# Optimization experiments

Hardware: AMD Instinct MI355X
Metric: run time of the kernel (lower is better)

Reference implementation:

```python
import jax, jax.numpy as jnp
import numpy as np

N = 50000
E = 600000
D_IN = 128
D_OUT = 128
EPS = 1e-12  # F.normalize eps


def setup_inputs() -> dict:
    key = jax.random.key(0)
    ks = jax.random.split(key, 10)
    s = 1.0 / np.sqrt(D_IN)
    inp = {
        "x": jax.random.normal(ks[0], (N, D_IN), dtype=jnp.float32),
        "edge_index": jax.random.randint(ks[1], (2, E), 0, N, dtype=jnp.int64),
        # conv1: lin_l (with bias) applied to aggregated neighbors, lin_r (no bias) to root
        "W1l": jax.random.uniform(ks[2], (D_IN, D_IN), jnp.float32, -s, s),
        "b1": jax.random.uniform(ks[3], (D_IN,), jnp.float32, -s, s),
        "W1r": jax.random.uniform(ks[4], (D_IN, D_IN), jnp.float32, -s, s),
        # conv2
        "W2l": jax.random.uniform(ks[5], (D_IN, D_OUT), jnp.float32, -s, s),
        "b2": jax.random.uniform(ks[6], (D_OUT,), jnp.float32, -s, s),
        "W2r": jax.random.uniform(ks[7], (D_IN, D_OUT), jnp.float32, -s, s),
        # final fc
        "Wf": jax.random.uniform(ks[8], (D_OUT, D_OUT), jnp.float32, -s, s),
        "bf": jax.random.uniform(ks[9], (D_OUT,), jnp.float32, -s, s),
    }
    return inp


def _sage_conv(x, src, dst, Wl, bl, Wr):
    # mean-aggregate messages from source nodes onto destination nodes
    msgs = x[src]  # [E, d] gather
    agg = jax.ops.segment_sum(msgs, dst, num_segments=N)  # [N, d]
    cnt = jax.ops.segment_sum(jnp.ones((src.shape[0],), x.dtype), dst, num_segments=N)
    agg = agg / jnp.maximum(cnt, 1.0)[:, None]  # isolated nodes -> 0
    out = agg @ Wl + bl + x @ Wr
    # L2 normalize per node (PyG normalize=True)
    nrm = jnp.sqrt(jnp.sum(out * out, axis=-1, keepdims=True))
    return out / jnp.maximum(nrm, EPS)


def reference(x, edge_index, W1l, b1, W1r, W2l, b2, W2r, Wf, bf):
    src, dst = edge_index[0], edge_index[1]
    h = jax.nn.relu(_sage_conv(x, src, dst, W1l, b1, W1r))
    h = jax.nn.relu(_sage_conv(h, src, dst, W2l, b2, W2r))
    return h @ Wf + bf
```

## Files before the change

### kernel.cpp

```cpp
#include <hip/hip_runtime.h>
#include <hip/hip_fp16.h>

#define D 128
#define SCAN_B 256

typedef __attribute__((ext_vector_type(8))) _Float16 f16x8;
typedef __attribute__((ext_vector_type(4))) float f32x4;

typedef __attribute__((address_space(1))) const void gas_t;
typedef __attribute__((address_space(3))) void las_t;

__global__ void scan_pass1(const int* __restrict__ cnt, int* __restrict__ rs,
                           int* __restrict__ bsum, int N) {
    __shared__ int lds[SCAN_B];
    int tid = threadIdx.x;
    int i = blockIdx.x * SCAN_B + tid;
    int v = (i < N) ? cnt[i] : 0;
    lds[tid] = v;
    __syncthreads();
    for (int o = 1; o < SCAN_B; o <<= 1) {
        int t = (tid >= o) ? lds[tid - o] : 0;
        __syncthreads();
        lds[tid] += t;
        __syncthreads();
    }
    if (i < N) rs[i] = lds[tid] - v;
    if (tid == SCAN_B - 1) bsum[blockIdx.x] = lds[tid];
}

__global__ void scan_pass2(int* __restrict__ bsum, int nb) {
    __shared__ int lds[SCAN_B];
    int tid = threadIdx.x;
    int v = (tid < nb) ? bsum[tid] : 0;
    lds[tid] = v;
    __syncthreads();
    for (int o = 1; o < SCAN_B; o <<= 1) {
        int t = (tid >= o) ? lds[tid - o] : 0;
        __syncthreads();
        lds[tid] += t;
        __syncthreads();
    }
    if (tid < nb) bsum[tid] = lds[tid] - v;
}

__global__ void scan_pass3(int* __restrict__ rs, int* __restrict__ cursor,
                           const int* __restrict__ bsum, const int* __restrict__ cnt,
                           float* __restrict__ inv, int N) {
    int i = blockIdx.x * SCAN_B + threadIdx.x;
    if (i < N) {
        int v = rs[i] + bsum[blockIdx.x];
        rs[i] = v;
        cursor[i] = v;
        inv[i] = 1.0f / (float)max(cnt[i], 1);
    }
}

__global__ void fill_kernel(const int* __restrict__ ei, int E,
                            int* __restrict__ cursor, int* __restrict__ csr) {
    int e = blockIdx.x * blockDim.x + threadIdx.x;
    if (e < E) {
        int src = ei[e], dst = ei[E + e];
        int pos = atomicAdd(&cursor[dst], 1);
        csr[pos] = src;
    }
}

__global__ void prologue_kernel(const float* __restrict__ W1l, const float* __restrict__ W1r,
                                const float* __restrict__ W2l, const float* __restrict__ W2r,
                                const float* __restrict__ Wf, unsigned short* __restrict__ pw,
                                const float* __restrict__ x, __half* __restrict__ xh,
                                __half* __restrict__ xl, int n8,
                                const int* __restrict__ ei, int E, int* __restrict__ cnt) {
    int t = blockIdx.x * blockDim.x + threadIdx.x;
    if (t < 10240) {
        int idx = t;
        int w = idx >> 11;
        int r = idx & 2047;
        int ks = r >> 9;
        int tt = (r >> 6) & 7;
        int lane = r & 63;
        int q = lane >> 4, n = lane & 15;
        const float* W = (w == 0) ? W1l : (w == 1) ? W1r : (w == 2) ? W2l : (w == 3) ? W2r : Wf;
        unsigned short* dh = pw + (size_t)w * 32768;
        unsigned short* dl = dh + 16384;
        int off = ((ks * 8 + tt) * 64 + lane) * 8;
#pragma unroll
        for (int j = 0; j < 8; j++) {
            float v = W[(size_t)(ks * 32 + q * 8 + j) * D + tt * 16 + n];
            __half hb = __float2half_rn(v);
            dh[off + j] = __half_as_ushort(hb);
            dl[off + j] = __half_as_ushort(__float2half_rn(v - __half2float(hb)));
        }
    } else if (t < 10240 + n8) {
        int i = t - 10240;
        const float4* x4 = (const float4*)x;
        float4 a = x4[2 * i], b = x4[2 * i + 1];
        float v[8] = {a.x, a.y, a.z, a.w, b.x, b.y, b.z, b.w};
        uint4 oh, ol;
        __half2* ph = (__half2*)&oh;
        __half2* pl = (__half2*)&ol;
#pragma unroll
        for (int jj = 0; jj < 4; jj++) {
            __half h0 = __float2half_rn(v[2 * jj]);
            __half h1 = __float2half_rn(v[2 * jj + 1]);
            ph[jj] = __halves2half2(h0, h1);
            pl[jj] = __halves2half2(__float2half_rn(v[2 * jj] - __half2float(h0)),
                                    __float2half_rn(v[2 * jj + 1] - __half2float(h1)));
        }
        ((uint4*)xh)[i] = oh;
        ((uint4*)xl)[i] = ol;
    } else {
        int e = t - 10240 - n8;
        if (e < E) atomicAdd(&cnt[ei[E + e]], 1);
    }
}

__device__ __forceinline__ void acc8(uint4 v, float* s) {
    const __half2* h = reinterpret_cast<const __half2*>(&v);
    float2 f0 = __half22float2(h[0]);
    float2 f1 = __half22float2(h[1]);
    float2 f2 = __half22float2(h[2]);
    float2 f3 = __half22float2(h[3]);
    s[0] += f0.x; s[1] += f0.y; s[2] += f1.x; s[3] += f1.y;
    s[4] += f2.x; s[5] += f2.y; s[6] += f3.x; s[7] += f3.y;
}

__global__ void aggregate_kernel(const __half* __restrict__ xh, int sstride,
                                 const int* __restrict__ csr,
                                 const int* __restrict__ rs, const int* __restrict__ cnt,
                                 const float* __restrict__ inv,
                                 __half* __restrict__ aggh, __half* __restrict__ aggl, int N) {
    int t = blockIdx.x * blockDim.x + threadIdx.x;
    int node = t >> 4;
    int c = t & 15;
    if (node >= N) return;
    int deg = cnt[node];
    int st = rs[node];
    const uint4* x4 = (const uint4*)xh;
    float s[8] = {0.f, 0.f, 0.f, 0.f, 0.f, 0.f, 0.f, 0.f};
    int i = 0;
    for (; i + 4 <= deg; i += 4) {
        int n0 = csr[st + i + 0], n1 = csr[st + i + 1];
        int n2 = csr[st + i + 2], n3 = csr[st + i + 3];
        uint4 v0 = x4[(size_t)n0 * sstride + c];
        uint4 v1 = x4[(size_t)n1 * sstride + c];
        uint4 v2 = x4[(size_t)n2 * sstride + c];
        uint4 v3 = x4[(size_t)n3 * sstride + c];
        acc8(v0, s); acc8(v1, s); acc8(v2, s); acc8(v3, s);
    }
    for (; i < deg; i++) {
        int n0 = csr[st + i];
        uint4 v0 = x4[(size_t)n0 * sstride + c];
        acc8(v0, s);
    }
    float iv = inv[node];
    uint4 oh, ol;
    __half2* ph = (__half2*)&oh;
    __half2* pl = (__half2*)&ol;
#pragma unroll
    for (int jj = 0; jj < 4; jj++) {
        float v0 = s[2 * jj] * iv, v1 = s[2 * jj + 1] * iv;
        __half h0 = __float2half_rn(v0), h1 = __float2half_rn(v1);
        ph[jj] = __halves2half2(h0, h1);
        pl[jj] = __halves2half2(__float2half_rn(v0 - __half2float(h0)),
                                __float2half_rn(v1 - __half2float(h1)));
    }
    ((uint4*)aggh)[(size_t)node * 16 + c] = oh;
    ((uint4*)aggl)[(size_t)node * 16 + c] = ol;
}

template <int LAYER>
__global__ __launch_bounds__(256) void mfma_gemm(
        const uint4* __restrict__ Agh, const uint4* __restrict__ Agl,
        const uint4* __restrict__ Ah1, const uint4* __restrict__ Al1,
        const uint4* __restrict__ W0h, const uint4* __restrict__ W0l,
        const uint4* __restrict__ W1h, const uint4* __restrict__ W1l,
        const float* __restrict__ bias,
        const uint4* __restrict__ W2h, const uint4* __restrict__ W2l,
        const float* __restrict__ bias2,
        float* out, __half* Hout, int N) {
    __shared__ uint4 smem4[2048];

    const int tid = threadIdx.x;
    const int lane = tid & 63;
    const int wave = tid >> 6;
    const int c = lane & 15;
    const int q = lane >> 4;
    const int R = blockIdx.x * 64 + wave * 16;
    const int row0 = min(R + c, N - 1);
    const size_t rb16 = (size_t)row0 * 16 + q;
    const size_t rbA1 = (size_t)row0 * (LAYER == 1 ? 16 : 32) + q;

#define STAGE_W(ks_, b_)                                                                   \
    do {                                                                                   \
        const uint4* sh_ = (((ks_) < 4) ? W0h : W1h) + (size_t)((ks_) & 3) * 512;          \
        const uint4* sl_ = (((ks_) < 4) ? W0l : W1l) + (size_t)((ks_) & 3) * 512;          \
        const uint4* s_ = ((wave < 2) ? sh_ : sl_) + ((wave & 1) * 256 + lane);            \
        uint4* d_ = smem4 + (b_) * 1024 + (wave >> 1) * 512 + (wave & 1) * 256;            \
        __builtin_amdgcn_global_load_lds((gas_t*)(s_), (las_t*)(d_), 16, 0, 0);            \
        __builtin_amdgcn_global_load_lds((gas_t*)(s_ + 64), (las_t*)(d_ + 64), 16, 0, 0);  \
        __builtin_amdgcn_global_load_lds((gas_t*)(s_ + 128), (las_t*)(d_ + 128), 16, 0, 0);\
        __builtin_amdgcn_global_load_lds((gas_t*)(s_ + 192), (las_t*)(d_ + 192), 16, 0, 0);\
    } while (0)

#define LOAD_A(ks_, s_)                                                       \
    do {                                                                      \
        if ((ks_) < 4) {                                                      \
            A_h[s_] = Agh[rb16 + (ks_) * 4];                                  \
            A_l[s_] = Agl[rb16 + (ks_) * 4];                                  \
        } else {                                                              \
            A_h[s_] = Ah1[rbA1 + ((ks_) - 4) * 4];                            \
            A_l[s_] = Al1[rbA1 + ((ks_) - 4) * 4];                            \
        }                                                                     \
    } while (0)

    uint4 A_h[2], A_l[2];
    STAGE_W(0, 0);
    STAGE_W(1, 1);
    LOAD_A(0, 0);
    LOAD_A(1, 1);
    asm volatile("s_waitcnt vmcnt(0)" ::: "memory");
    __syncthreads();

    f32x4 acc[8];
#pragma unroll
    for (int t = 0; t < 8; t++)
#pragma unroll
        for (int r = 0; r < 4; r++) acc[t][r] = 0.0f;

#pragma unroll
    for (int ks = 0; ks < 8; ks++) {
        const int b = ks & 1;
        const uint4* wb = smem4 + b * 1024;
        f16x8 ah = __builtin_bit_cast(f16x8, A_h[b]);
        f16x8 al = __builtin_bit_cast(f16x8, A_l[b]);
#pragma unroll
        for (int t = 0; t < 8; t++) {
            f16x8 bh = __builtin_bit_cast(f16x8, wb[t * 64 + lane]);
            f16x8 bl = __builtin_bit_cast(f16x8, wb[512 + t * 64 + lane]);
            acc[t] = __builtin_amdgcn_mfma_f32_16x16x32_f16(ah, bh, acc[t], 0, 0, 0);
            acc[t] = __builtin_amdgcn_mfma_f32_16x16x32_f16(al, bh, acc[t], 0, 0, 0);
            acc[t] = __builtin_amdgcn_mfma_f32_16x16x32_f16(ah, bl, acc[t], 0, 0, 0);
        }
        if (ks < 7) {
            asm volatile("s_waitcnt vmcnt(0)" ::: "memory");
            __syncthreads();
            if (ks < 6) {
                STAGE_W(ks + 2, b);
                LOAD_A(ks + 2, b);
            }
        }
    }

#pragma unroll
    for (int t = 0; t < 8; t++) {
        float bv = bias[t * 16 + c];
#pragma unroll
        for (int r = 0; r < 4; r++) acc[t][r] += bv;
    }
#pragma unroll
    for (int r = 0; r < 4; r++) {
        float v = 0.0f;
#pragma unroll
        for (int t = 0; t < 8; t++) v += acc[t][r] * acc[t][r];
        v += __shfl_xor(v, 1, 16);
        v += __shfl_xor(v, 2, 16);
        v += __shfl_xor(v, 4, 16);
        v += __shfl_xor(v, 8, 16);
        float rn = 1.0f / fmaxf(sqrtf(v), 1e-12f);
#pragma unroll
        for (int t = 0; t < 8; t++) acc[t][r] = fmaxf(acc[t][r] * rn, 0.0f);
    }

    if (LAYER == 1) {
#pragma unroll
        for (int t = 0; t < 8; t++)
#pragma unroll
            for (int r = 0; r < 4; r++) {
                int row = R + q * 4 + r;
                if (row < N) {
                    float v = acc[t][r];
                    __half h = __float2half_rn(v);
                    size_t base = (size_t)row * 256;
                    Hout[base + t * 16 + c] = h;
                    Hout[base + 128 + t * 16 + c] = __float2half_rn(v - __half2float(h));
                }
            }
        return;
    }

    __syncthreads();
    unsigned short* hw = (unsigned short*)(smem4 + wave * 512);
#pragma unroll
    for (int t = 0; t < 8; t++)
#pragma unroll
        for (int r = 0; r < 4; r++) {
            int m = q * 4 + r;
            float v = acc[t][r];
            __half h = __float2half_rn(v);
            int j4 = (t * 2 + (c >> 3)) ^ (m & 7);
            int off = m * 128 + j4 * 8 + (c & 7);
            hw[off] = __half_as_ushort(h);
            hw[2048 + off] = __half_as_ushort(__float2half_rn(v - __half2float(h)));
        }
    uint4 a2h_[4], a2l_[4];
#pragma unroll
    for (int k2 = 0; k2 < 4; k2++) {
        int r4 = (k2 * 4 + q) ^ (c & 7);
        a2h_[k2] = *(const uint4*)(hw + c * 128 + r4 * 8);
        a2l_[k2] = *(const uint4*)(hw + 2048 + c * 128 + r4 * 8);
    }

    f32x4 acc2[8];
#pragma unroll
    for (int t = 0; t < 8; t++) {
        float bv = bias2[t * 16 + c];
#pragma unroll
        for (int r = 0; r < 4; r++) acc2[t][r] = bv;
    }
#pragma unroll
    for (int k2 = 0; k2 < 4; k2++) {
        const uint4* Wh = W2h + (size_t)k2 * 512 + lane;
        const uint4* Wl = W2l + (size_t)k2 * 512 + lane;
        f16x8 ah = __builtin_bit_cast(f16x8, a2h_[k2]);
        f16x8 al = __builtin_bit_cast(f16x8, a2l_[k2]);
#pragma unroll
        for (int t = 0; t < 8; t++) {
            f16x8 bh = __builtin_bit_cast(f16x8, Wh[t * 64]);
            f16x8 bl = __builtin_bit_cast(f16x8, Wl[t * 64]);
            acc2[t] = __builtin_amdgcn_mfma_f32_16x16x32_f16(ah, bh, acc2[t], 0, 0, 0);
            acc2[t] = __builtin_amdgcn_mfma_f32_16x16x32_f16(al, bh, acc2[t], 0, 0, 0);
            acc2[t] = __builtin_amdgcn_mfma_f32_16x16x32_f16(ah, bl, acc2[t], 0, 0, 0);
        }
    }

#pragma unroll
    for (int t = 0; t < 8; t++)
#pragma unroll
        for (int r = 0; r < 4; r++) {
            int row = R + q * 4 + r;
            if (row < N) out[(size_t)row * D + t * 16 + c] = acc2[t][r];
        }
#undef STAGE_W
#undef LOAD_A
}

extern "C" void kernel_launch(void* const* d_in, const int* in_sizes, int n_in,
                              void* d_out, int out_size, void* d_ws, size_t ws_size,
                              hipStream_t stream) {
    const float* x   = (const float*)d_in[0];
    const int*   ei  = (const int*)d_in[1];
    const float* W1l = (const float*)d_in[2];
    const float* b1  = (const float*)d_in[3];
    const float* W1r = (const float*)d_in[4];
    const float* W2l = (const float*)d_in[5];
    const float* b2  = (const float*)d_in[6];
    const float* W2r = (const float*)d_in[7];
    const float* Wf  = (const float*)d_in[8];
    const float* bf  = (const float*)d_in[9];
    float* out = (float*)d_out;

    int N = in_sizes[0] / D;
    int E = in_sizes[1] / 2;

    __half* Agh = (__half*)d_ws;
    __half* Agl = Agh + (size_t)N * D;
    __half* Xh  = Agl + (size_t)N * D;
    __half* Xl  = Xh + (size_t)N * D;
    float* inv  = (float*)(Xl + (size_t)N * D);
    int*   rs     = (int*)(inv + N);
    int*   cnt    = rs + N;
    int*   cursor = cnt + N;
    int*   bsum   = cursor + N;
    int*   csr    = bsum + 256;
    unsigned short* pw = (unsigned short*)(csr + E);
    unsigned short* p1lh = pw + 0 * 32768, *p1ll = p1lh + 16384;
    unsigned short* p1rh = pw + 1 * 32768, *p1rl = p1rh + 16384;
    unsigned short* p2lh = pw + 2 * 32768, *p2ll = p2lh + 16384;
    unsigned short* p2rh = pw + 3 * 32768, *p2rl = p2rh + 16384;
    unsigned short* pfh  = pw + 4 * 32768, *pfl  = pfh + 16384;

    __half* H1 = (__half*)d_out;

    int nb = (N + SCAN_B - 1) / SCAN_B;
    int n8 = N * 16;

    hipMemsetAsync(cnt, 0, (size_t)N * sizeof(int), stream);
    int pro_threads = 10240 + n8 + E;
    prologue_kernel<<<(pro_threads + 255) / 256, 256, 0, stream>>>(
        W1l, W1r, W2l, W2r, Wf, pw, x, Xh, Xl, n8, ei, E, cnt);
    scan_pass1<<<nb, SCAN_B, 0, stream>>>(cnt, rs, bsum, N);
    scan_pass2<<<1, SCAN_B, 0, stream>>>(bsum, nb);
    scan_pass3<<<nb, SCAN_B, 0, stream>>>(rs, cursor, bsum, cnt, inv, N);
    fill_kernel<<<(E + 255) / 256, 256, 0, stream>>>(ei, E, cursor, csr);

    int agg_blocks = (N * 16 + 255) / 256;
    int gemm_blocks = (N + 63) / 64;

    aggregate_kernel<<<agg_blocks, 256, 0, stream>>>(Xh, 16, csr, rs, cnt, inv, Agh, Agl, N);
    mfma_gemm<1><<<gemm_blocks, 256, 0, stream>>>(
        (const uint4*)Agh, (const uint4*)Agl, (const uint4*)Xh, (const uint4*)Xl,
        (const uint4*)p1lh, (const uint4*)p1ll, (const uint4*)p1rh, (const uint4*)p1rl, b1,
        nullptr, nullptr, nullptr, nullptr, H1, N);

    aggregate_kernel<<<agg_blocks, 256, 0, stream>>>(H1, 32, csr, rs, cnt, inv, Agh, Agl, N);
    mfma_gemm<2><<<gemm_blocks, 256, 0, stream>>>(
        (const uint4*)Agh, (const uint4*)Agl,
        (const uint4*)d_out, (const uint4*)d_out + 16,
        (const uint4*)p2lh, (const uint4*)p2ll, (const uint4*)p2rh, (const uint4*)p2rl, b2,
        (const uint4*)pfh, (const uint4*)pfl, bf, out, nullptr, N);
}
```

Baseline: 261.0 us.

## Fuse neighbor mean aggregation into the MFMA GEMM kernels

Removes the separate aggregate kernels and instead has each GEMM lane gather and average its row's neighbor features directly into registers, split into hi/lo fp16, before the MFMA loop. This drops the write and re-read of the aggregated Agh/Agl buffers and two kernel launches. H1 moves from the output buffer into workspace. The trade-off is that each node's gather is now spread over only 4 lanes per row with 16-byte strided loads, leaving far fewer threads for the irregular gather. It also raises register pressure, because 32 float accumulators plus 16 uint4 operands are held per lane.

```diff
diff --git a/kernel.cpp b/kernel.cpp
--- a/kernel.cpp
+++ b/kernel.cpp
@@ -125,53 +125,24 @@
     s[4] += f2.x; s[5] += f2.y; s[6] += f3.x; s[7] += f3.y;
 }
 
-__global__ void aggregate_kernel(const __half* __restrict__ xh, int sstride,
-                                 const int* __restrict__ csr,
-                                 const int* __restrict__ rs, const int* __restrict__ cnt,
-                                 const float* __restrict__ inv,
-                                 __half* __restrict__ aggh, __half* __restrict__ aggl, int N) {
-    int t = blockIdx.x * blockDim.x + threadIdx.x;
-    int node = t >> 4;
-    int c = t & 15;
-    if (node >= N) return;
-    int deg = cnt[node];
-    int st = rs[node];
-    const uint4* x4 = (const uint4*)xh;
-    float s[8] = {0.f, 0.f, 0.f, 0.f, 0.f, 0.f, 0.f, 0.f};
-    int i = 0;
-    for (; i + 4 <= deg; i += 4) {
-        int n0 = csr[st + i + 0], n1 = csr[st + i + 1];
-        int n2 = csr[st + i + 2], n3 = csr[st + i + 3];
-        uint4 v0 = x4[(size_t)n0 * sstride + c];
-        uint4 v1 = x4[(size_t)n1 * sstride + c];
-        uint4 v2 = x4[(size_t)n2 * sstride + c];
-        uint4 v3 = x4[(size_t)n3 * sstride + c];
-        acc8(v0, s); acc8(v1, s); acc8(v2, s); acc8(v3, s);
-    }
-    for (; i < deg; i++) {
-        int n0 = csr[st + i];
-        uint4 v0 = x4[(size_t)n0 * sstride + c];
-        acc8(v0, s);
-    }
-    float iv = inv[node];
-    uint4 oh, ol;
-    __half2* ph = (__half2*)&oh;
-    __half2* pl = (__half2*)&ol;
+__device__ __forceinline__ void split_f16(const float* v, uint4& hi, uint4& lo) {
+    __half2* ph = (__half2*)&hi;
+    __half2* pl = (__half2*)&lo;
 #pragma unroll
     for (int jj = 0; jj < 4; jj++) {
-        float v0 = s[2 * jj] * iv, v1 = s[2 * jj + 1] * iv;
-        __half h0 = __float2half_rn(v0), h1 = __float2half_rn(v1);
+        __half h0 = __float2half_rn(v[2 * jj]);
+        __half h1 = __float2half_rn(v[2 * jj + 1]);
         ph[jj] = __halves2half2(h0, h1);
-        pl[jj] = __halves2half2(__float2half_rn(v0 - __half2float(h0)),
-                                __float2half_rn(v1 - __half2float(h1)));
-    }
-    ((uint4*)aggh)[(size_t)node * 16 + c] = oh;
-    ((uint4*)aggl)[(size_t)node * 16 + c] = ol;
+        pl[jj] = __halves2half2(__float2half_rn(v[2 * jj] - __half2float(h0)),
+                                __float2half_rn(v[2 * jj + 1] - __half2float(h1)));
+    }
 }
 
 template <int LAYER>
-__global__ __launch_bounds__(256) void mfma_gemm(
-        const uint4* __restrict__ Agh, const uint4* __restrict__ Agl,
+__global__ __launch_bounds__(256) void fused_gemm(
+        const int* __restrict__ csr, const int* __restrict__ rs,
+        const int* __restrict__ cnt, const float* __restrict__ inv,
+        const uint4* __restrict__ Gsrc,
         const uint4* __restrict__ Ah1, const uint4* __restrict__ Al1,
         const uint4* __restrict__ W0h, const uint4* __restrict__ W0l,
         const uint4* __restrict__ W1h, const uint4* __restrict__ W1l,
@@ -180,6 +151,7 @@
         const float* __restrict__ bias2,
         float* out, __half* Hout, int N) {
     __shared__ uint4 smem4[2048];
+    const int GS = (LAYER == 1) ? 16 : 32;
 
     const int tid = threadIdx.x;
     const int lane = tid & 63;
@@ -188,8 +160,7 @@
     const int q = lane >> 4;
     const int R = blockIdx.x * 64 + wave * 16;
     const int row0 = min(R + c, N - 1);
-    const size_t rb16 = (size_t)row0 * 16 + q;
-    const size_t rbA1 = (size_t)row0 * (LAYER == 1 ? 16 : 32) + q;
+    const size_t rbA1 = (size_t)row0 * GS + q;
 
 #define STAGE_W(ks_, b_)                                                                   \
     do {                                                                                   \
@@ -203,22 +174,50 @@
         __builtin_amdgcn_global_load_lds((gas_t*)(s_ + 192), (las_t*)(d_ + 192), 16, 0, 0);\
     } while (0)
 
-#define LOAD_A(ks_, s_)                                                       \
-    do {                                                                      \
-        if ((ks_) < 4) {                                                      \
-            A_h[s_] = Agh[rb16 + (ks_) * 4];                                  \
-            A_l[s_] = Agl[rb16 + (ks_) * 4];                                  \
-        } else {                                                              \
-            A_h[s_] = Ah1[rbA1 + ((ks_) - 4) * 4];                            \
-            A_l[s_] = Al1[rbA1 + ((ks_) - 4) * 4];                            \
-        }                                                                     \
-    } while (0)
-
-    uint4 A_h[2], A_l[2];
     STAGE_W(0, 0);
     STAGE_W(1, 1);
-    LOAD_A(0, 0);
-    LOAD_A(1, 1);
+    uint4 Xs_h[4], Xs_l[4];
+#pragma unroll
+    for (int kl = 0; kl < 4; kl++) {
+        Xs_h[kl] = Ah1[rbA1 + kl * 4];
+        Xs_l[kl] = Al1[rbA1 + kl * 4];
+    }
+
+    int deg = cnt[row0];
+    int st = rs[row0];
+    float iv = inv[row0];
+    float s[4][8];
+#pragma unroll
+    for (int ks = 0; ks < 4; ks++)
+#pragma unroll
+        for (int j = 0; j < 8; j++) s[ks][j] = 0.0f;
+
+    int i = 0;
+    for (; i + 2 <= deg; i += 2) {
+        int n0 = csr[st + i], n1 = csr[st + i + 1];
+        const uint4* g0 = Gsrc + (size_t)n0 * GS + q;
+        const uint4* g1 = Gsrc + (size_t)n1 * GS + q;
+        uint4 a0 = g0[0], a1 = g0[4], a2 = g0[8], a3 = g0[12];
+        uint4 b0 = g1[0], b1 = g1[4], b2 = g1[8], b3 = g1[12];
+        acc8(a0, s[0]); acc8(a1, s[1]); acc8(a2, s[2]); acc8(a3, s[3]);
+        acc8(b0, s[0]); acc8(b1, s[1]); acc8(b2, s[2]); acc8(b3, s[3]);
+    }
+    if (i < deg) {
+        int n0 = csr[st + i];
+        const uint4* g0 = Gsrc + (size_t)n0 * GS + q;
+        uint4 a0 = g0[0], a1 = g0[4], a2 = g0[8], a3 = g0[12];
+        acc8(a0, s[0]); acc8(a1, s[1]); acc8(a2, s[2]); acc8(a3, s[3]);
+    }
+
+    uint4 Agg_h[4], Agg_l[4];
+#pragma unroll
+    for (int ks = 0; ks < 4; ks++) {
+        float v[8];
+#pragma unroll
+        for (int j = 0; j < 8; j++) v[j] = s[ks][j] * iv;
+        split_f16(v, Agg_h[ks], Agg_l[ks]);
+    }
+
     asm volatile("s_waitcnt vmcnt(0)" ::: "memory");
     __syncthreads();
 
@@ -232,8 +231,8 @@
     for (int ks = 0; ks < 8; ks++) {
         const int b = ks & 1;
         const uint4* wb = smem4 + b * 1024;
-        f16x8 ah = __builtin_bit_cast(f16x8, A_h[b]);
-        f16x8 al = __builtin_bit_cast(f16x8, A_l[b]);
+        f16x8 ah = __builtin_bit_cast(f16x8, (ks < 4) ? Agg_h[ks & 3] : Xs_h[ks & 3]);
+        f16x8 al = __builtin_bit_cast(f16x8, (ks < 4) ? Agg_l[ks & 3] : Xs_l[ks & 3]);
 #pragma unroll
         for (int t = 0; t < 8; t++) {
             f16x8 bh = __builtin_bit_cast(f16x8, wb[t * 64 + lane]);
@@ -245,10 +244,7 @@
         if (ks < 7) {
             asm volatile("s_waitcnt vmcnt(0)" ::: "memory");
             __syncthreads();
-            if (ks < 6) {
-                STAGE_W(ks + 2, b);
-                LOAD_A(ks + 2, b);
-            }
+            if (ks < 6) STAGE_W(ks + 2, b);
         }
     }
 
@@ -342,7 +338,6 @@
             if (row < N) out[(size_t)row * D + t * 16 + c] = acc2[t][r];
         }
 #undef STAGE_W
-#undef LOAD_A
 }
 
 extern "C" void kernel_launch(void* const* d_in, const int* in_sizes, int n_in,
@@ -363,11 +358,10 @@
     int N = in_sizes[0] / D;
     int E = in_sizes[1] / 2;
 
-    __half* Agh = (__half*)d_ws;
-    __half* Agl = Agh + (size_t)N * D;
-    __half* Xh  = Agl + (size_t)N * D;
+    __half* Xh  = (__half*)d_ws;
     __half* Xl  = Xh + (size_t)N * D;
-    float* inv  = (float*)(Xl + (size_t)N * D);
+    __half* H1  = Xl + (size_t)N * D;
+    float* inv  = (float*)(H1 + (size_t)N * 256);
     int*   rs     = (int*)(inv + N);
     int*   cnt    = rs + N;
     int*   cursor = cnt + N;
@@ -380,8 +374,6 @@
     unsigned short* p2rh = pw + 3 * 32768, *p2rl = p2rh + 16384;
     unsigned short* pfh  = pw + 4 * 32768, *pfl  = pfh + 16384;
 
-    __half* H1 = (__half*)d_out;
-
     int nb = (N + SCAN_B - 1) / SCAN_B;
     int n8 = N * 16;
 
@@ -394,19 +386,17 @@
     scan_pass3<<<nb, SCAN_B, 0, stream>>>(rs, cursor, bsum, cnt, inv, N);
     fill_kernel<<<(E + 255) / 256, 256, 0, stream>>>(ei, E, cursor, csr);
 
-    int agg_blocks = (N * 16 + 255) / 256;
     int gemm_blocks = (N + 63) / 64;
 
-    aggregate_kernel<<<agg_blocks, 256, 0, stream>>>(Xh, 16, csr, rs, cnt, inv, Agh, Agl, N);
-    mfma_gemm<1><<<gemm_blocks, 256, 0, stream>>>(
-        (const uint4*)Agh, (const uint4*)Agl, (const uint4*)Xh, (const uint4*)Xl,
+    fused_gemm<1><<<gemm_blocks, 256, 0, stream>>>(
+        csr, rs, cnt, inv,
+        (const uint4*)Xh, (const uint4*)Xh, (const uint4*)Xl,
         (const uint4*)p1lh, (const uint4*)p1ll, (const uint4*)p1rh, (const uint4*)p1rl, b1,
         nullptr, nullptr, nullptr, nullptr, H1, N);
 
-    aggregate_kernel<<<agg_blocks, 256, 0, stream>>>(H1, 32, csr, rs, cnt, inv, Agh, Agl, N);
-    mfma_gemm<2><<<gemm_blocks, 256, 0, stream>>>(
-        (const uint4*)Agh, (const uint4*)Agl,
-        (const uint4*)d_out, (const uint4*)d_out + 16,
+    fused_gemm<2><<<gemm_blocks, 256, 0, stream>>>(
+        csr, rs, cnt, inv,
+        (const uint4*)H1, (const uint4*)H1, (const uint4*)H1 + 16,
         (const uint4*)p2lh, (const uint4*)p2ll, (const uint4*)p2rh, (const uint4*)p2rl, b2,
         (const uint4*)pfh, (const uint4*)pfl, bf, out, nullptr, N);
 }
```

New measurement: 271.8 us. 4.2% more time.

## Deepen GEMM weight staging, LDS-stage final FC weights, merge scan passes

Applied to the files above, without the earlier changes.

The layer GEMM now stages two k-steps of weights and A fragments per barrier, using a 64KB LDS buffer. This halves the number of sync points in the main loop. The final FC weights, previously read straight from global memory, are now double-buffered into LDS with async loads that overlap the H transpose. The separate block-sum scan kernel is folded into scan_pass3: each block redundantly scans the block sums, which saves one launch but repeats the small scan in every block. The larger LDS footprint may lower occupancy.

```diff
diff --git a/kernel.cpp b/kernel.cpp
--- a/kernel.cpp
+++ b/kernel.cpp
@@ -28,7 +28,9 @@
     if (tid == SCAN_B - 1) bsum[blockIdx.x] = lds[tid];
 }
 
-__global__ void scan_pass2(int* __restrict__ bsum, int nb) {
+__global__ void scan_pass3(int* __restrict__ rs, int* __restrict__ cursor,
+                           const int* __restrict__ bsum, const int* __restrict__ cnt,
+                           float* __restrict__ inv, int N, int nb) {
     __shared__ int lds[SCAN_B];
     int tid = threadIdx.x;
     int v = (tid < nb) ? bsum[tid] : 0;
@@ -40,17 +42,12 @@
         lds[tid] += t;
         __syncthreads();
     }
-    if (tid < nb) bsum[tid] = lds[tid] - v;
-}
-
-__global__ void scan_pass3(int* __restrict__ rs, int* __restrict__ cursor,
-                           const int* __restrict__ bsum, const int* __restrict__ cnt,
-                           float* __restrict__ inv, int N) {
-    int i = blockIdx.x * SCAN_B + threadIdx.x;
+    int boff = (blockIdx.x == 0) ? 0 : lds[blockIdx.x - 1];
+    int i = blockIdx.x * SCAN_B + tid;
     if (i < N) {
-        int v = rs[i] + bsum[blockIdx.x];
-        rs[i] = v;
-        cursor[i] = v;
+        int vv = rs[i] + boff;
+        rs[i] = vv;
+        cursor[i] = vv;
         inv[i] = 1.0f / (float)max(cnt[i], 1);
     }
 }
@@ -179,7 +176,7 @@
         const uint4* __restrict__ W2h, const uint4* __restrict__ W2l,
         const float* __restrict__ bias2,
         float* out, __half* Hout, int N) {
-    __shared__ uint4 smem4[2048];
+    __shared__ uint4 smem4[4096];
 
     const int tid = threadIdx.x;
     const int lane = tid & 63;
@@ -191,12 +188,12 @@
     const size_t rb16 = (size_t)row0 * 16 + q;
     const size_t rbA1 = (size_t)row0 * (LAYER == 1 ? 16 : 32) + q;
 
-#define STAGE_W(ks_, b_)                                                                   \
+#define STAGE_W(ks_, o_)                                                                   \
     do {                                                                                   \
         const uint4* sh_ = (((ks_) < 4) ? W0h : W1h) + (size_t)((ks_) & 3) * 512;          \
         const uint4* sl_ = (((ks_) < 4) ? W0l : W1l) + (size_t)((ks_) & 3) * 512;          \
         const uint4* s_ = ((wave < 2) ? sh_ : sl_) + ((wave & 1) * 256 + lane);            \
-        uint4* d_ = smem4 + (b_) * 1024 + (wave >> 1) * 512 + (wave & 1) * 256;            \
+        uint4* d_ = smem4 + (o_) + (wave >> 1) * 512 + (wave & 1) * 256;                   \
         __builtin_amdgcn_global_load_lds((gas_t*)(s_), (las_t*)(d_), 16, 0, 0);            \
         __builtin_amdgcn_global_load_lds((gas_t*)(s_ + 64), (las_t*)(d_ + 64), 16, 0, 0);  \
         __builtin_amdgcn_global_load_lds((gas_t*)(s_ + 128), (las_t*)(d_ + 128), 16, 0, 0);\
@@ -214,11 +211,15 @@
         }                                                                     \
     } while (0)
 
-    uint4 A_h[2], A_l[2];
+    uint4 A_h[4], A_l[4];
     STAGE_W(0, 0);
-    STAGE_W(1, 1);
+    STAGE_W(1, 1024);
+    STAGE_W(2, 2048);
+    STAGE_W(3, 3072);
     LOAD_A(0, 0);
     LOAD_A(1, 1);
+    LOAD_A(2, 2);
+    LOAD_A(3, 3);
     asm volatile("s_waitcnt vmcnt(0)" ::: "memory");
     __syncthreads();
 
@@ -229,25 +230,30 @@
         for (int r = 0; r < 4; r++) acc[t][r] = 0.0f;
 
 #pragma unroll
-    for (int ks = 0; ks < 8; ks++) {
-        const int b = ks & 1;
-        const uint4* wb = smem4 + b * 1024;
-        f16x8 ah = __builtin_bit_cast(f16x8, A_h[b]);
-        f16x8 al = __builtin_bit_cast(f16x8, A_l[b]);
-#pragma unroll
-        for (int t = 0; t < 8; t++) {
-            f16x8 bh = __builtin_bit_cast(f16x8, wb[t * 64 + lane]);
-            f16x8 bl = __builtin_bit_cast(f16x8, wb[512 + t * 64 + lane]);
-            acc[t] = __builtin_amdgcn_mfma_f32_16x16x32_f16(ah, bh, acc[t], 0, 0, 0);
-            acc[t] = __builtin_amdgcn_mfma_f32_16x16x32_f16(al, bh, acc[t], 0, 0, 0);
-            acc[t] = __builtin_amdgcn_mfma_f32_16x16x32_f16(ah, bl, acc[t], 0, 0, 0);
-        }
-        if (ks < 7) {
+    for (int kp = 0; kp < 4; kp++) {
+        const int b = kp & 1;
+#pragma unroll
+        for (int s = 0; s < 2; s++) {
+            const uint4* wb = smem4 + b * 2048 + s * 1024;
+            f16x8 ah = __builtin_bit_cast(f16x8, A_h[b * 2 + s]);
+            f16x8 al = __builtin_bit_cast(f16x8, A_l[b * 2 + s]);
+#pragma unroll
+            for (int t = 0; t < 8; t++) {
+                f16x8 bh = __builtin_bit_cast(f16x8, wb[t * 64 + lane]);
+                f16x8 bl = __builtin_bit_cast(f16x8, wb[512 + t * 64 + lane]);
+                acc[t] = __builtin_amdgcn_mfma_f32_16x16x32_f16(ah, bh, acc[t], 0, 0, 0);
+                acc[t] = __builtin_amdgcn_mfma_f32_16x16x32_f16(al, bh, acc[t], 0, 0, 0);
+                acc[t] = __builtin_amdgcn_mfma_f32_16x16x32_f16(ah, bl, acc[t], 0, 0, 0);
+            }
+        }
+        if (kp < 3) {
             asm volatile("s_waitcnt vmcnt(0)" ::: "memory");
             __syncthreads();
-            if (ks < 6) {
-                STAGE_W(ks + 2, b);
-                LOAD_A(ks + 2, b);
+            if (kp < 2) {
+                STAGE_W(2 * kp + 4, b * 2048);
+                STAGE_W(2 * kp + 5, b * 2048 + 1024);
+                LOAD_A(2 * kp + 4, b * 2 + 0);
+                LOAD_A(2 * kp + 5, b * 2 + 1);
             }
         }
     }
@@ -290,7 +296,22 @@
     }
 
     __syncthreads();
-    unsigned short* hw = (unsigned short*)(smem4 + wave * 512);
+
+#define STAGE_F(k2_, b_)                                                                   \
+    do {                                                                                   \
+        const uint4* s_ = ((wave < 2) ? W2h : W2l) + (size_t)(k2_) * 512 +                 \
+                          (wave & 1) * 256 + lane;                                         \
+        uint4* d_ = smem4 + (b_) * 1024 + (wave >> 1) * 512 + (wave & 1) * 256;            \
+        __builtin_amdgcn_global_load_lds((gas_t*)(s_), (las_t*)(d_), 16, 0, 0);            \
+        __builtin_amdgcn_global_load_lds((gas_t*)(s_ + 64), (las_t*)(d_ + 64), 16, 0, 0);  \
+        __builtin_amdgcn_global_load_lds((gas_t*)(s_ + 128), (las_t*)(d_ + 128), 16, 0, 0);\
+        __builtin_amdgcn_global_load_lds((gas_t*)(s_ + 192), (las_t*)(d_ + 192), 16, 0, 0);\
+    } while (0)
+
+    STAGE_F(0, 0);
+    STAGE_F(1, 1);
+
+    unsigned short* hw = (unsigned short*)(smem4 + 2048 + wave * 512);
 #pragma unroll
     for (int t = 0; t < 8; t++)
 #pragma unroll
@@ -311,6 +332,9 @@
         a2l_[k2] = *(const uint4*)(hw + 2048 + c * 128 + r4 * 8);
     }
 
+    asm volatile("s_waitcnt vmcnt(0)" ::: "memory");
+    __syncthreads();
+
     f32x4 acc2[8];
 #pragma unroll
     for (int t = 0; t < 8; t++) {
@@ -320,18 +344,23 @@
     }
 #pragma unroll
     for (int k2 = 0; k2 < 4; k2++) {
-        const uint4* Wh = W2h + (size_t)k2 * 512 + lane;
-        const uint4* Wl = W2l + (size_t)k2 * 512 + lane;
+        const int b = k2 & 1;
+        const uint4* wb2 = smem4 + b * 1024;
         f16x8 ah = __builtin_bit_cast(f16x8, a2h_[k2]);
         f16x8 al = __builtin_bit_cast(f16x8, a2l_[k2]);
 #pragma unroll
         for (int t = 0; t < 8; t++) {
-            f16x8 bh = __builtin_bit_cast(f16x8, Wh[t * 64]);
-            f16x8 bl = __builtin_bit_cast(f16x8, Wl[t * 64]);
+            f16x8 bh = __builtin_bit_cast(f16x8, wb2[t * 64 + lane]);
+            f16x8 bl = __builtin_bit_cast(f16x8, wb2[512 + t * 64 + lane]);
             acc2[t] = __builtin_amdgcn_mfma_f32_16x16x32_f16(ah, bh, acc2[t], 0, 0, 0);
             acc2[t] = __builtin_amdgcn_mfma_f32_16x16x32_f16(al, bh, acc2[t], 0, 0, 0);
             acc2[t] = __builtin_amdgcn_mfma_f32_16x16x32_f16(ah, bl, acc2[t], 0, 0, 0);
         }
+        if (k2 < 3) {
+            asm volatile("s_waitcnt vmcnt(0)" ::: "memory");
+            __syncthreads();
+            if (k2 < 2) STAGE_F(k2 + 2, b);
+        }
     }
 
 #pragma unroll
@@ -342,6 +371,7 @@
             if (row < N) out[(size_t)row * D + t * 16 + c] = acc2[t][r];
         }
 #undef STAGE_W
+#undef STAGE_F
 #undef LOAD_A
 }
 
@@ -390,8 +420,7 @@
     prologue_kernel<<<(pro_threads + 255) / 256, 256, 0, stream>>>(
         W1l, W1r, W2l, W2r, Wf, pw, x, Xh, Xl, n8, ei, E, cnt);
     scan_pass1<<<nb, SCAN_B, 0, stream>>>(cnt, rs, bsum, N);
-    scan_pass2<<<1, SCAN_B, 0, stream>>>(bsum, nb);
-    scan_pass3<<<nb, SCAN_B, 0, stream>>>(rs, cursor, bsum, cnt, inv, N);
+    scan_pass3<<<nb, SCAN_B, 0, stream>>>(rs, cursor, bsum, cnt, inv, N, nb);
     fill_kernel<<<(E + 255) / 256, 256, 0, stream>>>(ei, E, cursor, csr);
 
     int agg_blocks = (N * 16 + 255) / 256;
```

After: 260.3 us. About the same (-0.2%).

## Fuse block-sum scan into pass3 and preload all A fragments in GEMM

Applied to the files above, without the earlier changes.

Removes the single-block scan_pass2 launch by having every pass3 block redundantly scan the block sums in LDS and pick its own offset. In the GEMM, all eight A-operand fragments are loaded into registers up front instead of being double-buffered per k-step, so only weight staging stays in the loop. Launch bounds now declare a minimum of one block per CU, which gives the compiler a larger register budget. The extra registers may reduce occupancy, and each pass3 block repeats a small scan.

```diff
diff --git a/kernel.cpp b/kernel.cpp
--- a/kernel.cpp
+++ b/kernel.cpp
@@ -28,7 +28,9 @@
     if (tid == SCAN_B - 1) bsum[blockIdx.x] = lds[tid];
 }
 
-__global__ void scan_pass2(int* __restrict__ bsum, int nb) {
+__global__ void scan_pass3(int* __restrict__ rs, int* __restrict__ cursor,
+                           const int* __restrict__ bsum, const int* __restrict__ cnt,
+                           float* __restrict__ inv, int N, int nb) {
     __shared__ int lds[SCAN_B];
     int tid = threadIdx.x;
     int v = (tid < nb) ? bsum[tid] : 0;
@@ -40,17 +42,12 @@
         lds[tid] += t;
         __syncthreads();
     }
-    if (tid < nb) bsum[tid] = lds[tid] - v;
-}
-
-__global__ void scan_pass3(int* __restrict__ rs, int* __restrict__ cursor,
-                           const int* __restrict__ bsum, const int* __restrict__ cnt,
-                           float* __restrict__ inv, int N) {
-    int i = blockIdx.x * SCAN_B + threadIdx.x;
+    int boff = (blockIdx.x == 0) ? 0 : lds[blockIdx.x - 1];
+    int i = blockIdx.x * SCAN_B + tid;
     if (i < N) {
-        int v = rs[i] + bsum[blockIdx.x];
-        rs[i] = v;
-        cursor[i] = v;
+        int vv = rs[i] + boff;
+        rs[i] = vv;
+        cursor[i] = vv;
         inv[i] = 1.0f / (float)max(cnt[i], 1);
     }
 }
@@ -170,7 +167,7 @@
 }
 
 template <int LAYER>
-__global__ __launch_bounds__(256) void mfma_gemm(
+__global__ __launch_bounds__(256, 1) void mfma_gemm(
         const uint4* __restrict__ Agh, const uint4* __restrict__ Agl,
         const uint4* __restrict__ Ah1, const uint4* __restrict__ Al1,
         const uint4* __restrict__ W0h, const uint4* __restrict__ W0l,
@@ -203,22 +200,16 @@
         __builtin_amdgcn_global_load_lds((gas_t*)(s_ + 192), (las_t*)(d_ + 192), 16, 0, 0);\
     } while (0)
 
-#define LOAD_A(ks_, s_)                                                       \
-    do {                                                                      \
-        if ((ks_) < 4) {                                                      \
-            A_h[s_] = Agh[rb16 + (ks_) * 4];                                  \
-            A_l[s_] = Agl[rb16 + (ks_) * 4];                                  \
-        } else {                                                              \
-            A_h[s_] = Ah1[rbA1 + ((ks_) - 4) * 4];                            \
-            A_l[s_] = Al1[rbA1 + ((ks_) - 4) * 4];                            \
-        }                                                                     \
-    } while (0)
-
-    uint4 A_h[2], A_l[2];
+    uint4 A_h[8], A_l[8];
+#pragma unroll
+    for (int kl = 0; kl < 4; kl++) {
+        A_h[kl] = Agh[rb16 + kl * 4];
+        A_l[kl] = Agl[rb16 + kl * 4];
+        A_h[4 + kl] = Ah1[rbA1 + kl * 4];
+        A_l[4 + kl] = Al1[rbA1 + kl * 4];
+    }
     STAGE_W(0, 0);
     STAGE_W(1, 1);
-    LOAD_A(0, 0);
-    LOAD_A(1, 1);
     asm volatile("s_waitcnt vmcnt(0)" ::: "memory");
     __syncthreads();
 
@@ -232,8 +223,8 @@
     for (int ks = 0; ks < 8; ks++) {
         const int b = ks & 1;
         const uint4* wb = smem4 + b * 1024;
-        f16x8 ah = __builtin_bit_cast(f16x8, A_h[b]);
-        f16x8 al = __builtin_bit_cast(f16x8, A_l[b]);
+        f16x8 ah = __builtin_bit_cast(f16x8, A_h[ks]);
+        f16x8 al = __builtin_bit_cast(f16x8, A_l[ks]);
 #pragma unroll
         for (int t = 0; t < 8; t++) {
             f16x8 bh = __builtin_bit_cast(f16x8, wb[t * 64 + lane]);
@@ -245,10 +236,7 @@
         if (ks < 7) {
             asm volatile("s_waitcnt vmcnt(0)" ::: "memory");
             __syncthreads();
-            if (ks < 6) {
-                STAGE_W(ks + 2, b);
-                LOAD_A(ks + 2, b);
-            }
+            if (ks < 6) STAGE_W(ks + 2, b);
         }
     }
 
@@ -342,7 +330,6 @@
             if (row < N) out[(size_t)row * D + t * 16 + c] = acc2[t][r];
         }
 #undef STAGE_W
-#undef LOAD_A
 }
 
 extern "C" void kernel_launch(void* const* d_in, const int* in_sizes, int n_in,
@@ -390,8 +377,7 @@
     prologue_kernel<<<(pro_threads + 255) / 256, 256, 0, stream>>>(
         W1l, W1r, W2l, W2r, Wf, pw, x, Xh, Xl, n8, ei, E, cnt);
     scan_pass1<<<nb, SCAN_B, 0, stream>>>(cnt, rs, bsum, N);
-    scan_pass2<<<1, SCAN_B, 0, stream>>>(bsum, nb);
-    scan_pass3<<<nb, SCAN_B, 0, stream>>>(rs, cursor, bsum, cnt, inv, N);
+    scan_pass3<<<nb, SCAN_B, 0, stream>>>(rs, cursor, bsum, cnt, inv, N, nb);
     fill_kernel<<<(E + 255) / 256, 256, 0, stream>>>(ei, E, cursor, csr);
 
     int agg_blocks = (N * 16 + 255) / 256;
```

Result: no change. 266.0 us (+1.9%).
